# Kernel optimization log

Measured on AMD Instinct MI355X. Metric: run time of the kernel, lower is better.

The kernel has to match this reference:

```python
import jax, jax.numpy as jnp
import numpy as np

CS = 64          # chunk_size
CP = CS - 1      # causal_padding
H = 8            # heads
DH = 64          # dim_head
SCALE = DH ** -0.5


def rotate_half(x):
    x1, x2 = jnp.split(x, 2, axis=-1)
    return jnp.concatenate((-x2, x1), axis=-1)


def apply_rope(t, freqs):
    rd = freqs.shape[-1]
    t_rot, t_pass = t[..., :rd], t[..., rd:]
    t_rot = t_rot * jnp.cos(freqs) + rotate_half(t_rot) * jnp.sin(freqs)
    return jnp.concatenate((t_rot, t_pass), axis=-1)


def setup_inputs() -> dict:
    key = jax.random.key(0)
    ks = jax.random.split(key, 10)
    b, n, dim = 4, 4096, 1024
    k_chunks, r, rlen = 64, 2, 128
    inner = H * DH
    return {
        "x": jax.random.normal(ks[0], (b, n, dim), dtype=jnp.float32),
        "context": jax.random.normal(ks[1], (b, k_chunks, r, rlen, dim), dtype=jnp.float32),
        "q_pos_emb": jax.random.normal(ks[2], (1, 1, CS, DH), dtype=jnp.float32),
        "k_pos_emb": jax.random.normal(ks[3], (1, 1, rlen, DH), dtype=jnp.float32),
        "Wq": jax.random.normal(ks[4], (dim, inner), dtype=jnp.float32) * 0.02,
        "Wk": jax.random.normal(ks[5], (dim, inner), dtype=jnp.float32) * 0.02,
        "Wv": jax.random.normal(ks[6], (dim, inner), dtype=jnp.float32) * 0.02,
        "Wo": jax.random.normal(ks[7], (inner, dim), dtype=jnp.float32) * 0.02,
        "bo": jnp.zeros((dim,), dtype=jnp.float32),
        "null_k": jax.random.normal(ks[8], (inner,), dtype=jnp.float32),
        "null_v": jax.random.normal(ks[9], (inner,), dtype=jnp.float32),
    }


def reference(x, context, q_pos_emb, k_pos_emb, Wq, Wk, Wv, Wo, bo, null_k, null_v):
    b, n, dim = x.shape
    _, k_chunks, r, rlen, _ = context.shape
    # causal shift: drop first CP tokens, pad CP zeros at end (F.pad with -CP)
    xs = jnp.pad(x[:, CP:], ((0, 0), (0, CP), (0, 0)))
    seq_index = (n // CS) * CS
    rem = n - seq_index
    xs = xs[:, :seq_index]                                   # [b, k*CS, dim]
    # shift q rope the same way; pad region gets freqs=0 -> identity rotation
    qpe = jnp.pad(q_pos_emb[:, :, CP:], ((0, 0), (0, 0), (0, CP), (0, 0)))
    kpe = jnp.tile(k_pos_emb, (1, 1, r, 1))                  # [1,1,r*rlen,DH]
    bk = b * k_chunks
    xc = xs.reshape(bk, CS, dim)
    ctx = context.reshape(bk, r * rlen, dim)
    # projections -> [bk, h, seq, dh]
    q = (xc @ Wq).reshape(bk, CS, H, DH).transpose(0, 2, 1, 3) * SCALE
    k = (ctx @ Wk).reshape(bk, r * rlen, H, DH).transpose(0, 2, 1, 3)
    v = (ctx @ Wv).reshape(bk, r * rlen, H, DH).transpose(0, 2, 1, 3)
    q = apply_rope(q, qpe)
    k = apply_rope(k, kpe)
    # null kv prepend
    nk = jnp.broadcast_to(null_k.reshape(1, H, 1, DH), (bk, H, 1, DH))
    nv = jnp.broadcast_to(null_v.reshape(1, H, 1, DH), (bk, H, 1, DH))
    k = jnp.concatenate((nk, k), axis=2)
    v = jnp.concatenate((nv, v), axis=2)
    sim = jnp.einsum('bhid,bhjd->bhij', q, k)
    attn = jax.nn.softmax(sim, axis=-1)
    o = jnp.einsum('bhij,bhjd->bhid', attn, v)
    o = o.transpose(0, 2, 1, 3).reshape(bk, CS, H * DH)
    o = o @ Wo + bo                                          # [bk, CS, dim]
    o = o.reshape(b, k_chunks * CS, dim)
    # unshift: pad CP zeros at front, trim CP - rem from end
    o = jnp.concatenate(
        (jnp.zeros((b, CP, dim), o.dtype), o[:, :k_chunks * CS - CP + rem]), axis=1)
    return o
```

## Files before the change

### kernel.cpp

```cpp
#include <hip/hip_runtime.h>


#define DEV __device__ __forceinline__

typedef __bf16 bf16x8 __attribute__((ext_vector_type(8)));
typedef float f32x4 __attribute__((ext_vector_type(4)));

DEV unsigned short f2bf(float f) {
  union { float f; unsigned int u; } v; v.f = f;
  unsigned int u = v.u;
  unsigned int r = (u + 0x7FFFu + ((u >> 16) & 1u)) >> 16;
  return (unsigned short)r;
}
DEV float bf2f(unsigned short h) {
  union { unsigned int u; float f; } v; v.u = ((unsigned int)h) << 16;
  return v.f;
}
DEV unsigned int pkbf(unsigned int hi, unsigned int lo) {
  return __builtin_amdgcn_perm(hi, lo, 0x07060302u);
}

DEV void ldst16(const void* g, void* l) {
  __builtin_amdgcn_global_load_lds(
      (const __attribute__((address_space(1))) void*)g,
      (__attribute__((address_space(3))) void*)l, 16, 0, 0);
}

DEV void bar() { __builtin_amdgcn_s_barrier(); }
#define VMCNT4 asm volatile("s_waitcnt vmcnt(4)" ::: "memory")
#define VMCNT0 asm volatile("s_waitcnt vmcnt(0)" ::: "memory")

__global__ __launch_bounds__(256) void prep_k(const float* __restrict__ Wq,
                                              const float* __restrict__ Wk,
                                              const float* __restrict__ Wv,
                                              const float* __restrict__ Wo,
                                              const float* __restrict__ qpe,
                                              const float* __restrict__ kpe,
                                              unsigned short* __restrict__ Wqt,
                                              unsigned short* __restrict__ Wkt,
                                              unsigned short* __restrict__ Wvt,
                                              unsigned short* __restrict__ Wot,
                                              float* __restrict__ ck, float* __restrict__ sk,
                                              float* __restrict__ cq, float* __restrict__ sq,
                                              float* __restrict__ out) {
  __shared__ float tl[64][65];
  int blk = blockIdx.x;
  int tid = threadIdx.x;
  if (blk < 512) {
    int mat = blk >> 7, loc = blk & 127;
    const float* W;
    unsigned short* Wt;
    int R, C;
    float scale = 1.0f;
    if (mat == 0)      { W = Wq; Wt = Wqt; R = 1024; C = 512; scale = 0.125f; }
    else if (mat == 1) { W = Wk; Wt = Wkt; R = 1024; C = 512; }
    else if (mat == 2) { W = Wv; Wt = Wvt; R = 1024; C = 512; }
    else               { W = Wo; Wt = Wot; R = 512;  C = 1024; }
    int nct = C >> 6;
    int rt = loc / nct, ct = loc % nct;
    int r0 = rt << 6, c0 = ct << 6;
    #pragma unroll
    for (int i = 0; i < 16; ++i) {
      int flat = i * 256 + tid;
      int rr = flat >> 6, cc = flat & 63;
      tl[rr][cc] = W[(size_t)(r0 + rr) * C + c0 + cc] * scale;
    }
    __syncthreads();
    #pragma unroll
    for (int i = 0; i < 16; ++i) {
      int flat = i * 256 + tid;
      int cc = flat >> 6, rr = flat & 63;
      Wt[(size_t)(c0 + cc) * R + r0 + rr] = f2bf(tl[rr][cc]);
    }
  } else if (blk < 764) {
    int r = blk - 512;
    int b = r / 63, rr = r % 63;
    float4 z = {0.f, 0.f, 0.f, 0.f};
    *(float4*)(out + (((size_t)(b * 4096 + rr)) << 10) + tid * 4) = z;
  } else {
    int t = (blk - 764) * 256 + tid;
    float f = kpe[t];
    ck[t] = cosf(f);
    sk[t] = sinf(f);
    if (t < 64) {
      float g = qpe[63 * 64 + t];
      cq[t] = cosf(g);
      sq[t] = sinf(g);
    }
  }
}

__global__ __launch_bounds__(256) void cast_k(const float* __restrict__ src,
                                              unsigned short* __restrict__ dst) {
  size_t base = ((size_t)blockIdx.x * 256 + threadIdx.x) * 8;
  uint4 lo = *(const uint4*)(src + base);
  uint4 hi = *(const uint4*)(src + base + 4);
  uint4 pk;
  pk.x = pkbf(lo.y, lo.x);
  pk.y = pkbf(lo.w, lo.z);
  pk.z = pkbf(hi.y, hi.x);
  pk.w = pkbf(hi.w, hi.z);
  *(uint4*)(dst + base) = pk;
}

template <int MODE>
__global__ __launch_bounds__(256) void gemm_proj(const float* __restrict__ Af,
                                                 const unsigned short* __restrict__ B0,
                                                 const unsigned short* __restrict__ B1,
                                                 unsigned short* __restrict__ out0,
                                                 unsigned short* __restrict__ out1,
                                                 const float* __restrict__ ck,
                                                 const float* __restrict__ sk,
                                                 const float* __restrict__ cq,
                                                 const float* __restrict__ sq) {
  __shared__ unsigned short sh[16384];
  unsigned short* As = sh;
  unsigned short* Bs = sh + 8192;
  const int K = 1024;

  int id = blockIdx.x;
  int x, y, z;
  if (MODE == 0) { x = (id & 7) + 8 * (id >> 5); y = (id >> 3) & 3; z = 0; }
  else           { x = (id & 7) + 8 * (id >> 6); int j = (id >> 3) & 7; y = j & 3; z = j >> 2; }
  const unsigned short* B = z ? B1 : B0;
  int m0 = x * 128, n0 = y * 128;
  int tid = threadIdx.x, w = tid >> 6, lane = tid & 63;
  int wm = (w & 1) * 64, wn = (w >> 1) * 64;
  int Lrow = lane >> 3, Lc = lane & 7;
  int srcC = Lc ^ (Lrow & 7);

  const float* asrc[4];
  bool avalid[4];
  #pragma unroll
  for (int q = 0; q < 4; ++q) {
    int t = w * 4 + q;
    int gm = m0 + t * 8 + Lrow;
    if (MODE == 0) {
      int b = gm >> 12, p = gm & 4095;
      avalid[q] = (p <= 4032);
      asrc[q] = Af + (((size_t)(b << 12) + p + 63) << 10) + srcC * 8;
    } else {
      avalid[q] = true;
      asrc[q] = Af + (size_t)gm * 1024 + srcC * 8;
    }
  }

  f32x4 acc[4][4] = {};

  for (int k0 = 0; k0 < K; k0 += 64) {
    #pragma unroll
    for (int q = 0; q < 4; ++q) {
      int t = w * 4 + q;
      uint4 lo = {0, 0, 0, 0}, hi = {0, 0, 0, 0};
      if (avalid[q]) {
        lo = *(const uint4*)(asrc[q] + k0);
        hi = *(const uint4*)(asrc[q] + k0 + 4);
      }
      uint4 pk;
      pk.x = pkbf(lo.y, lo.x);
      pk.y = pkbf(lo.w, lo.z);
      pk.z = pkbf(hi.y, hi.x);
      pk.w = pkbf(hi.w, hi.z);
      *(uint4*)((char*)As + t * 1024 + lane * 16) = pk;
      ldst16(B + (size_t)(n0 + t * 8 + Lrow) * K + (k0 + srcC * 8), (char*)Bs + t * 1024);
    }
    __syncthreads();
    #pragma unroll
    for (int k32 = 0; k32 < 2; ++k32) {
      int c = k32 * 4 + (lane >> 4);
      bf16x8 af[4], bfr[4];
      #pragma unroll
      for (int mt = 0; mt < 4; ++mt) {
        int m = wm + mt * 16 + (lane & 15);
        af[mt] = *(const bf16x8*)((const char*)As + m * 128 + (c ^ (m & 7)) * 16);
      }
      #pragma unroll
      for (int nt = 0; nt < 4; ++nt) {
        int n = wn + nt * 16 + (lane & 15);
        bfr[nt] = *(const bf16x8*)((const char*)Bs + n * 128 + (c ^ (n & 7)) * 16);
      }
      #pragma unroll
      for (int mt = 0; mt < 4; ++mt)
        #pragma unroll
        for (int nt = 0; nt < 4; ++nt)
          acc[mt][nt] = __builtin_amdgcn_mfma_f32_16x16x32_bf16(af[mt], bfr[nt], acc[mt][nt], 0, 0, 0);
    }
    __syncthreads();
  }

  if (MODE == 0) {
    #pragma unroll
    for (int mt = 0; mt < 4; ++mt)
      #pragma unroll
      for (int nt = 0; nt < 4; ++nt)
        #pragma unroll
        for (int r = 0; r < 4; ++r) {
          int m = m0 + wm + mt * 16 + (lane >> 4) * 4 + r;
          int n = n0 + wn + nt * 16 + (lane & 15);
          float val = acc[mt][nt][r];
          if ((m & 63) == 0) {
            int d = nt * 16 + (lane & 15);
            float partner = acc[mt][nt ^ 2][r];
            val = val * cq[d] + (nt < 2 ? -partner : partner) * sq[d];
          }
          out0[(size_t)m * 512 + n] = f2bf(val);
        }
  } else if (z == 0) {
    #pragma unroll
    for (int mt = 0; mt < 4; ++mt)
      #pragma unroll
      for (int r = 0; r < 4; ++r) {
        int m = m0 + wm + mt * 16 + (lane >> 4) * 4 + r;
        int fib = (m & 127) * 64;
        #pragma unroll
        for (int nt = 0; nt < 4; ++nt) {
          int n = n0 + wn + nt * 16 + (lane & 15);
          int d = nt * 16 + (lane & 15);
          float partner = acc[mt][nt ^ 2][r];
          float val = acc[mt][nt][r] * ck[fib + d] + (nt < 2 ? -partner : partner) * sk[fib + d];
          out0[(size_t)m * 512 + n] = f2bf(val);
        }
      }
  } else {
    #pragma unroll
    for (int mt = 0; mt < 4; ++mt)
      #pragma unroll
      for (int nt = 0; nt < 4; ++nt)
        #pragma unroll
        for (int r = 0; r < 4; ++r) {
          int ml = wm + mt * 16 + (lane >> 4) * 4 + r;
          int nl = wn + nt * 16 + (lane & 15);
          int mc = ml >> 3, me = ml & 7;
          *(unsigned short*)((char*)sh + nl * 256 + ((mc ^ (nl & 15)) * 16) + me * 2) =
              f2bf(acc[mt][nt][r]);
        }
    __syncthreads();
    #pragma unroll
    for (int i = 0; i < 8; ++i) {
      int flat = i * 256 + tid;
      int nl = flat >> 4, mc = flat & 15;
      uint4 v = *(const uint4*)((const char*)sh + nl * 256 + ((mc ^ (nl & 15)) * 16));
      *(uint4*)(out1 + (size_t)(n0 + nl) * 65536 + m0 + mc * 8) = v;
    }
  }
}

DEV bf16x8 rdfrag(const unsigned short* b, int row, int c) {
  return *(const bf16x8*)((const char*)b + row * 128 + ((c ^ (row & 7)) << 4));
}

DEV void rdA(const unsigned short* bufA, int wm, int ln15, int l4, int mtb,
             bf16x8 (&af)[2][2]) {
  #pragma unroll
  for (int mq = 0; mq < 2; ++mq)
    #pragma unroll
    for (int kk = 0; kk < 2; ++kk)
      af[mq][kk] = rdfrag(bufA, wm + (mtb + mq) * 16 + ln15, kk * 4 + l4);
}

DEV void rdB(const unsigned short* bufB, int wn, int ln15, int l4, bf16x8 (&bf)[4][2]) {
  #pragma unroll
  for (int nt = 0; nt < 4; ++nt)
    #pragma unroll
    for (int kk = 0; kk < 2; ++kk)
      bf[nt][kk] = rdfrag(bufB, wn + nt * 16 + ln15, kk * 4 + l4);
}

template <int MTB>
DEV void mfma16(const bf16x8 (&af)[2][2], const bf16x8 (&bf)[4][2], f32x4 (&acc)[8][4]) {
  __builtin_amdgcn_s_setprio(1);
  #pragma unroll
  for (int mq = 0; mq < 2; ++mq)
    #pragma unroll
    for (int nt = 0; nt < 4; ++nt)
      #pragma unroll
      for (int kk = 0; kk < 2; ++kk)
        acc[MTB + mq][nt] = __builtin_amdgcn_mfma_f32_16x16x32_bf16(
            af[mq][kk], bf[nt][kk], acc[MTB + mq][nt], 0, 0, 0);
  __builtin_amdgcn_s_setprio(0);
}

DEV void stg(unsigned short* buf, const unsigned short* src, int r0, int w,
             int Lrow, int srcC, int k0, int h) {
  #pragma unroll
  for (int qq = 0; qq < 2; ++qq) {
    int q = 2 * h + qq;
    ldst16(src + (size_t)(r0 + q * 64 + w * 8 + Lrow) * 1024 + (k0 + srcC * 8),
           (char*)buf + ((q * 512 + w * 64) << 4));
  }
}

__global__ __launch_bounds__(512, 2) void gemm_kv(const unsigned short* __restrict__ Abf,
                                                  const unsigned short* __restrict__ Bk,
                                                  const unsigned short* __restrict__ Bv,
                                                  unsigned short* __restrict__ kb,
                                                  unsigned short* __restrict__ vtg,
                                                  const float* __restrict__ ck,
                                                  const float* __restrict__ sk,
                                                  int mbase) {
  __shared__ unsigned short sh[65536];
  unsigned short* A0b = sh;
  unsigned short* A1b = sh + 16384;
  unsigned short* B0b = sh + 32768;
  unsigned short* B1b = sh + 49152;

  int id = blockIdx.x;
  int x = (id & 7) + 8 * (id >> 5);
  int j = (id >> 3) & 3;
  int y = j & 1, z = j >> 1;
  const unsigned short* Bz = z ? Bv : Bk;
  int m0l = x << 8;
  int m0 = mbase + m0l;
  int n0 = y << 8;

  int tid = threadIdx.x, w = tid >> 6, lane = tid & 63;
  int wm = (w & 1) * 128, wn = (w >> 1) * 64;
  int ln15 = lane & 15, l4 = lane >> 4;
  int Lrow = lane >> 3;
  int srcC = (lane & 7) ^ (Lrow & 7);

  f32x4 acc[8][4] = {};

  stg(A0b, Abf, m0l, w, Lrow, srcC, 0, 0);
  stg(A0b, Abf, m0l, w, Lrow, srcC, 0, 1);
  stg(B0b, Bz, n0, w, Lrow, srcC, 0, 0);
  stg(B0b, Bz, n0, w, Lrow, srcC, 0, 1);
  stg(B1b, Bz, n0, w, Lrow, srcC, 64, 0);
  stg(B1b, Bz, n0, w, Lrow, srcC, 64, 1);
  VMCNT4;
  bar();

  for (int it = 0; it < 8; ++it) {
    const int k0 = it * 128;
    bf16x8 af[2][2], bf[4][2];

    rdB(B0b, wn, ln15, l4, bf);
    rdA(A0b, wm, ln15, l4, 0, af);
    stg(A1b, Abf, m0l, w, Lrow, srcC, k0 + 64, 0);
    bar(); mfma16<0>(af, bf, acc); bar();

    rdA(A0b, wm, ln15, l4, 2, af);
    stg(A1b, Abf, m0l, w, Lrow, srcC, k0 + 64, 1);
    bar(); mfma16<2>(af, bf, acc); bar();

    rdA(A0b, wm, ln15, l4, 4, af);
    stg(B0b, Bz, n0, w, Lrow, srcC, (k0 + 128) & 1023, 0);
    bar(); mfma16<4>(af, bf, acc); bar();

    rdA(A0b, wm, ln15, l4, 6, af);
    stg(B0b, Bz, n0, w, Lrow, srcC, (k0 + 128) & 1023, 1);
    VMCNT4;
    bar(); mfma16<6>(af, bf, acc); bar();

    rdB(B1b, wn, ln15, l4, bf);
    rdA(A1b, wm, ln15, l4, 0, af);
    stg(A0b, Abf, m0l, w, Lrow, srcC, (k0 + 128) & 1023, 0);
    bar(); mfma16<0>(af, bf, acc); bar();

    rdA(A1b, wm, ln15, l4, 2, af);
    stg(A0b, Abf, m0l, w, Lrow, srcC, (k0 + 128) & 1023, 1);
    bar(); mfma16<2>(af, bf, acc); bar();

    rdA(A1b, wm, ln15, l4, 4, af);
    stg(B1b, Bz, n0, w, Lrow, srcC, (k0 + 192) & 1023, 0);
    bar(); mfma16<4>(af, bf, acc); bar();

    rdA(A1b, wm, ln15, l4, 6, af);
    stg(B1b, Bz, n0, w, Lrow, srcC, (k0 + 192) & 1023, 1);
    VMCNT4;
    bar(); mfma16<6>(af, bf, acc); bar();
  }

  VMCNT0;
  bar();

  if (z == 0) {
    #pragma unroll
    for (int mt = 0; mt < 8; ++mt)
      #pragma unroll
      for (int r = 0; r < 4; ++r) {
        int m = m0 + wm + mt * 16 + l4 * 4 + r;
        int fib = (m & 127) << 6;
        #pragma unroll
        for (int nt = 0; nt < 4; ++nt) {
          int d = nt * 16 + ln15;
          float partner = acc[mt][nt ^ 2][r];
          float val = acc[mt][nt][r] * ck[fib + d] + (nt < 2 ? -partner : partner) * sk[fib + d];
          kb[(size_t)m * 512 + n0 + wn + d] = f2bf(val);
        }
      }
  } else {
    #pragma unroll
    for (int mt = 0; mt < 8; ++mt)
      #pragma unroll
      for (int nt = 0; nt < 4; ++nt)
        #pragma unroll
        for (int r = 0; r < 4; ++r) {
          int ml = wm + mt * 16 + l4 * 4 + r;
          int nl = wn + nt * 16 + ln15;
          int mc = ml >> 3, me = ml & 7;
          *(unsigned short*)((char*)sh + nl * 512 + ((mc ^ (nl & 31)) << 4) + me * 2) =
              f2bf(acc[mt][nt][r]);
        }
    __syncthreads();
    #pragma unroll
    for (int i = 0; i < 16; ++i) {
      int flat = i * 512 + tid;
      int nl = flat >> 5, mc = flat & 31;
      uint4 v = *(const uint4*)((const char*)sh + nl * 512 + ((mc ^ (nl & 31)) << 4));
      *(uint4*)(vtg + (size_t)(n0 + nl) * 65536 + m0 + mc * 8) = v;
    }
  }
}

__global__ __launch_bounds__(256) void gemm_out(const unsigned short* __restrict__ A,
                                                const unsigned short* __restrict__ B,
                                                const float* __restrict__ bias,
                                                float* __restrict__ out) {
  __shared__ unsigned short sh[16384];
  unsigned short* As = sh;
  unsigned short* Bs = sh + 8192;
  const int K = 512, N = 1024;
  int id = blockIdx.x;
  int x = (id & 7) + 8 * (id >> 6), y = (id >> 3) & 7;
  int m0 = x * 128, n0 = y * 128;
  int tid = threadIdx.x, w = tid >> 6, lane = tid & 63;
  int wm = (w & 1) * 64, wn = (w >> 1) * 64;
  int Lrow = lane >> 3, Lc = lane & 7;
  int srcC = Lc ^ (Lrow & 7);

  f32x4 acc[4][4] = {};

  for (int k0 = 0; k0 < K; k0 += 64) {
    #pragma unroll
    for (int q = 0; q < 4; ++q) {
      int t = w * 4 + q;
      ldst16(A + (size_t)(m0 + t * 8 + Lrow) * K + (k0 + srcC * 8), (char*)As + t * 1024);
      ldst16(B + (size_t)(n0 + t * 8 + Lrow) * K + (k0 + srcC * 8), (char*)Bs + t * 1024);
    }
    __syncthreads();
    #pragma unroll
    for (int k32 = 0; k32 < 2; ++k32) {
      int c = k32 * 4 + (lane >> 4);
      bf16x8 af[4], bfr[4];
      #pragma unroll
      for (int mt = 0; mt < 4; ++mt) {
        int m = wm + mt * 16 + (lane & 15);
        af[mt] = *(const bf16x8*)((const char*)As + m * 128 + (c ^ (m & 7)) * 16);
      }
      #pragma unroll
      for (int nt = 0; nt < 4; ++nt) {
        int n = wn + nt * 16 + (lane & 15);
        bfr[nt] = *(const bf16x8*)((const char*)Bs + n * 128 + (c ^ (n & 7)) * 16);
      }
      #pragma unroll
      for (int mt = 0; mt < 4; ++mt)
        #pragma unroll
        for (int nt = 0; nt < 4; ++nt)
          acc[mt][nt] = __builtin_amdgcn_mfma_f32_16x16x32_bf16(af[mt], bfr[nt], acc[mt][nt], 0, 0, 0);
    }
    __syncthreads();
  }
  #pragma unroll
  for (int mt = 0; mt < 4; ++mt)
    #pragma unroll
    for (int nt = 0; nt < 4; ++nt)
      #pragma unroll
      for (int r = 0; r < 4; ++r) {
        int m = m0 + wm + mt * 16 + (lane >> 4) * 4 + r;
        int n = n0 + wn + nt * 16 + (lane & 15);
        int b = m >> 12, t = m & 4095;
        if (t <= 4032)
          out[((size_t)((b << 12) + t + 63)) * N + n] = acc[mt][nt][r] + bias[n];
      }
}

__global__ __launch_bounds__(256) void attn_kernel(const unsigned short* __restrict__ qb,
                                                   const unsigned short* __restrict__ kb,
                                                   const unsigned short* __restrict__ vtg,
                                                   const float* __restrict__ nullk,
                                                   const float* __restrict__ nullv,
                                                   unsigned short* __restrict__ ob) {
  __shared__ unsigned short qs[64 * 64];
  __shared__ unsigned short ks[256 * 64];
  __shared__ unsigned short ps[64 * 256];
  __shared__ float rnull[64];
  __shared__ float rsum[64];
  int id = blockIdx.x;
  int bc = (id & 7) + 8 * (id >> 6);
  int h = (id >> 3) & 7;
  int tid = threadIdx.x, w = tid >> 6, lane = tid & 63;
  int Lrow = lane >> 3, Lc = lane & 7, srcC = Lc ^ (Lrow & 7);

  #pragma unroll
  for (int q8 = 0; q8 < 2; ++q8) {
    int t = w * 2 + q8;
    ldst16(qb + (size_t)(bc * 64 + t * 8 + Lrow) * 512 + h * 64 + srcC * 8, (char*)qs + t * 1024);
  }
  #pragma unroll
  for (int q8 = 0; q8 < 8; ++q8) {
    int t = w * 8 + q8;
    ldst16(kb + (size_t)(bc * 256 + t * 8 + Lrow) * 512 + h * 64 + srcC * 8, (char*)ks + t * 1024);
  }
  __syncthreads();

  {
    int rl = lane >> 2, part = lane & 3;
    int row = w * 16 + rl;
    float s = 0.f;
    #pragma unroll
    for (int e = 0; e < 16; ++e) {
      int d = part * 16 + e;
      unsigned short qv = *(const unsigned short*)((const char*)qs + row * 128 +
                                                   (((d >> 3) ^ (row & 7)) * 16) + (d & 7) * 2);
      s += bf2f(qv) * nullk[h * 64 + d];
    }
    s += __shfl_xor(s, 1);
    s += __shfl_xor(s, 2);
    if (part == 0) rnull[row] = __expf(s);
  }

  f32x4 acc[16] = {};
  #pragma unroll
  for (int k32 = 0; k32 < 2; ++k32) {
    int c = k32 * 4 + (lane >> 4);
    int m = w * 16 + (lane & 15);
    bf16x8 a = *(const bf16x8*)((const char*)qs + m * 128 + (c ^ (m & 7)) * 16);
    #pragma unroll
    for (int nt = 0; nt < 16; ++nt) {
      int n = nt * 16 + (lane & 15);
      bf16x8 b = *(const bf16x8*)((const char*)ks + n * 128 + (c ^ (n & 7)) * 16);
      acc[nt] = __builtin_amdgcn_mfma_f32_16x16x32_bf16(a, b, acc[nt], 0, 0, 0);
    }
  }

  int g = lane >> 4;
  #pragma unroll
  for (int r = 0; r < 4; ++r) {
    int row = w * 16 + g * 4 + r;
    float s = 0.f;
    #pragma unroll
    for (int nt = 0; nt < 16; ++nt) {
      float p = __expf(acc[nt][r]);
      acc[nt][r] = p;
      s += p;
    }
    s += __shfl_xor(s, 1);
    s += __shfl_xor(s, 2);
    s += __shfl_xor(s, 4);
    s += __shfl_xor(s, 8);
    if ((lane & 15) == 0) rsum[row] = s + rnull[row];
  }

  #pragma unroll
  for (int nt = 0; nt < 16; ++nt)
    #pragma unroll
    for (int r = 0; r < 4; ++r) {
      int row = w * 16 + g * 4 + r;
      int col = nt * 16 + (lane & 15);
      *(unsigned short*)((char*)ps + row * 512 + (((col >> 3) ^ (row & 7)) * 16) + (col & 7) * 2) =
          f2bf(acc[nt][r]);
    }
  __syncthreads();

  #pragma unroll
  for (int q8 = 0; q8 < 8; ++q8) {
    int t = w * 8 + q8;
    int dd = t * 2 + (lane >> 5);
    int cl = (lane & 31) ^ (dd & 7);
    ldst16(vtg + (size_t)(h * 64 + dd) * 65536 + bc * 256 + cl * 8, (char*)ks + t * 1024);
  }
  __syncthreads();

  f32x4 oacc[4] = {};
  #pragma unroll
  for (int k32 = 0; k32 < 8; ++k32) {
    int c = k32 * 4 + (lane >> 4);
    int m = w * 16 + (lane & 15);
    bf16x8 a = *(const bf16x8*)((const char*)ps + m * 512 + (c ^ (m & 7)) * 16);
    #pragma unroll
    for (int nt = 0; nt < 4; ++nt) {
      int n = nt * 16 + (lane & 15);
      bf16x8 b = *(const bf16x8*)((const char*)ks + n * 512 + (c ^ (n & 7)) * 16);
      oacc[nt] = __builtin_amdgcn_mfma_f32_16x16x32_bf16(a, b, oacc[nt], 0, 0, 0);
    }
  }
  #pragma unroll
  for (int nt = 0; nt < 4; ++nt)
    #pragma unroll
    for (int r = 0; r < 4; ++r) {
      int row = w * 16 + g * 4 + r;
      int d = nt * 16 + (lane & 15);
      float o = oacc[nt][r] + rnull[row] * nullv[h * 64 + d];
      o /= rsum[row];
      ob[((size_t)(bc * 64 + row) * 8 + h) * 64 + d] = f2bf(o);
    }
}

extern "C" void kernel_launch(void* const* d_in, const int* in_sizes, int n_in,
                              void* d_out, int out_size, void* d_ws, size_t ws_size,
                              hipStream_t stream) {
  const float* x = (const float*)d_in[0];
  const float* ctx = (const float*)d_in[1];
  const float* qpe = (const float*)d_in[2];
  const float* kpe = (const float*)d_in[3];
  const float* Wq = (const float*)d_in[4];
  const float* Wk = (const float*)d_in[5];
  const float* Wv = (const float*)d_in[6];
  const float* Wo = (const float*)d_in[7];
  const float* bo = (const float*)d_in[8];
  const float* nk = (const float*)d_in[9];
  const float* nv = (const float*)d_in[10];
  float* out = (float*)d_out;
  char* ws = (char*)d_ws;

  unsigned short* Wqt  = (unsigned short*)(ws + 0);
  unsigned short* Wkt  = (unsigned short*)(ws + 1048576);
  unsigned short* Wvt  = (unsigned short*)(ws + 2097152);
  unsigned short* Wot  = (unsigned short*)(ws + 3145728);
  float* cosk = (float*)(ws + 4194304);
  float* sink = (float*)(ws + 4227072);
  float* cosq = (float*)(ws + 4259840);
  float* sinq = (float*)(ws + 4260096);
  unsigned short* qb   = (unsigned short*)(ws + 4260352);
  unsigned short* kb   = (unsigned short*)(ws + 21037568);
  unsigned short* vtg  = (unsigned short*)(ws + 88146432);
  unsigned short* obuf = (unsigned short*)(ws + 155255296);
  unsigned short* ctxb = (unsigned short*)(ws + 155255296);

  prep_k<<<796, 256, 0, stream>>>(Wq, Wk, Wv, Wo, qpe, kpe, Wqt, Wkt, Wvt, Wot,
                                  cosk, sink, cosq, sinq, out);

  gemm_proj<0><<<512, 256, 0, stream>>>(x, Wqt, Wqt, qb, nullptr,
                                        cosk, sink, cosq, sinq);

  cast_k<<<16384, 256, 0, stream>>>(ctx, ctxb);
  gemm_kv<<<512, 512, 0, stream>>>(ctxb, Wkt, Wvt, kb, vtg, cosk, sink, 0);
  cast_k<<<16384, 256, 0, stream>>>(ctx + 33554432, ctxb);
  gemm_kv<<<512, 512, 0, stream>>>(ctxb, Wkt, Wvt, kb, vtg, cosk, sink, 32768);

  attn_kernel<<<2048, 256, 0, stream>>>(qb, kb, vtg, nk, nv, obuf);

  gemm_out<<<1024, 256, 0, stream>>>(obuf, Wot, bo, out);
}
```

Baseline: 708.5 us.

## Merge Q/K/V projections into one pipelined GEMM and restructure attention

Casts all of context and shifted x to bf16 in one kernel. Q, K and V projections then run in a single launch that uses the double-buffered 256x256 tile loop from the old K/V GEMM, and the output projection moves to that same loop, replacing the smaller 128x128 single-buffer GEMMs. The attention kernel is reorganised so each lane owns one query row: it computes K·Q transposed, keeps the row sum and null-key terms in registers instead of shared memory, stages V in its own buffer, and writes packed outputs. This trades the extra bf16 staging traffic for x and all of context at once, plus a larger workspace, for fewer launches and better MFMA pipelining.

```diff
diff --git a/kernel.cpp b/kernel.cpp
--- a/kernel.cpp
+++ b/kernel.cpp
@@ -16,8 +16,15 @@
   union { unsigned int u; float f; } v; v.u = ((unsigned int)h) << 16;
   return v.f;
 }
+DEV float bfelem(bf16x8 v, int i) {
+  union { bf16x8 v; unsigned short u[8]; } t; t.v = v;
+  return bf2f(t.u[i]);
+}
 DEV unsigned int pkbf(unsigned int hi, unsigned int lo) {
   return __builtin_amdgcn_perm(hi, lo, 0x07060302u);
+}
+DEV unsigned int pk2(float lo, float hi) {
+  return ((unsigned int)f2bf(hi) << 16) | f2bf(lo);
 }
 
 DEV void ldst16(const void* g, void* l) {
@@ -90,163 +97,44 @@
   }
 }
 
-__global__ __launch_bounds__(256) void cast_k(const float* __restrict__ src,
-                                              unsigned short* __restrict__ dst) {
-  size_t base = ((size_t)blockIdx.x * 256 + threadIdx.x) * 8;
-  uint4 lo = *(const uint4*)(src + base);
-  uint4 hi = *(const uint4*)(src + base + 4);
-  uint4 pk;
-  pk.x = pkbf(lo.y, lo.x);
-  pk.y = pkbf(lo.w, lo.z);
-  pk.z = pkbf(hi.y, hi.x);
-  pk.w = pkbf(hi.w, hi.z);
-  *(uint4*)(dst + base) = pk;
-}
-
-template <int MODE>
-__global__ __launch_bounds__(256) void gemm_proj(const float* __restrict__ Af,
-                                                 const unsigned short* __restrict__ B0,
-                                                 const unsigned short* __restrict__ B1,
-                                                 unsigned short* __restrict__ out0,
-                                                 unsigned short* __restrict__ out1,
-                                                 const float* __restrict__ ck,
-                                                 const float* __restrict__ sk,
-                                                 const float* __restrict__ cq,
-                                                 const float* __restrict__ sq) {
-  __shared__ unsigned short sh[16384];
-  unsigned short* As = sh;
-  unsigned short* Bs = sh + 8192;
-  const int K = 1024;
-
+__global__ __launch_bounds__(256) void cast_all(const float* __restrict__ ctx,
+                                                const float* __restrict__ x,
+                                                unsigned short* __restrict__ ctxb,
+                                                unsigned short* __restrict__ xb) {
   int id = blockIdx.x;
-  int x, y, z;
-  if (MODE == 0) { x = (id & 7) + 8 * (id >> 5); y = (id >> 3) & 3; z = 0; }
-  else           { x = (id & 7) + 8 * (id >> 6); int j = (id >> 3) & 7; y = j & 3; z = j >> 2; }
-  const unsigned short* B = z ? B1 : B0;
-  int m0 = x * 128, n0 = y * 128;
-  int tid = threadIdx.x, w = tid >> 6, lane = tid & 63;
-  int wm = (w & 1) * 64, wn = (w >> 1) * 64;
-  int Lrow = lane >> 3, Lc = lane & 7;
-  int srcC = Lc ^ (Lrow & 7);
-
-  const float* asrc[4];
-  bool avalid[4];
-  #pragma unroll
-  for (int q = 0; q < 4; ++q) {
-    int t = w * 4 + q;
-    int gm = m0 + t * 8 + Lrow;
-    if (MODE == 0) {
-      int b = gm >> 12, p = gm & 4095;
-      avalid[q] = (p <= 4032);
-      asrc[q] = Af + (((size_t)(b << 12) + p + 63) << 10) + srcC * 8;
-    } else {
-      avalid[q] = true;
-      asrc[q] = Af + (size_t)gm * 1024 + srcC * 8;
-    }
-  }
-
-  f32x4 acc[4][4] = {};
-
-  for (int k0 = 0; k0 < K; k0 += 64) {
-    #pragma unroll
-    for (int q = 0; q < 4; ++q) {
-      int t = w * 4 + q;
-      uint4 lo = {0, 0, 0, 0}, hi = {0, 0, 0, 0};
-      if (avalid[q]) {
-        lo = *(const uint4*)(asrc[q] + k0);
-        hi = *(const uint4*)(asrc[q] + k0 + 4);
-      }
-      uint4 pk;
+  if (id < 32768) {
+    size_t base = ((size_t)id * 256 + threadIdx.x) * 8;
+    uint4 lo = *(const uint4*)(ctx + base);
+    uint4 hi = *(const uint4*)(ctx + base + 4);
+    uint4 pk;
+    pk.x = pkbf(lo.y, lo.x);
+    pk.y = pkbf(lo.w, lo.z);
+    pk.z = pkbf(hi.y, hi.x);
+    pk.w = pkbf(hi.w, hi.z);
+    *(uint4*)(ctxb + base) = pk;
+  } else {
+    size_t e = ((size_t)(id - 32768) * 256 + threadIdx.x) * 8;
+    int m = (int)(e >> 10), c = (int)(e & 1023);
+    int b = m >> 12, t = m & 4095;
+    uint4 pk = {0, 0, 0, 0};
+    if (t <= 4032) {
+      const float* s = x + (((size_t)(b << 12) + t + 63) << 10) + c;
+      uint4 lo = *(const uint4*)s;
+      uint4 hi = *(const uint4*)(s + 4);
       pk.x = pkbf(lo.y, lo.x);
       pk.y = pkbf(lo.w, lo.z);
       pk.z = pkbf(hi.y, hi.x);
       pk.w = pkbf(hi.w, hi.z);
-      *(uint4*)((char*)As + t * 1024 + lane * 16) = pk;
-      ldst16(B + (size_t)(n0 + t * 8 + Lrow) * K + (k0 + srcC * 8), (char*)Bs + t * 1024);
-    }
-    __syncthreads();
-    #pragma unroll
-    for (int k32 = 0; k32 < 2; ++k32) {
-      int c = k32 * 4 + (lane >> 4);
-      bf16x8 af[4], bfr[4];
-      #pragma unroll
-      for (int mt = 0; mt < 4; ++mt) {
-        int m = wm + mt * 16 + (lane & 15);
-        af[mt] = *(const bf16x8*)((const char*)As + m * 128 + (c ^ (m & 7)) * 16);
-      }
-      #pragma unroll
-      for (int nt = 0; nt < 4; ++nt) {
-        int n = wn + nt * 16 + (lane & 15);
-        bfr[nt] = *(const bf16x8*)((const char*)Bs + n * 128 + (c ^ (n & 7)) * 16);
-      }
-      #pragma unroll
-      for (int mt = 0; mt < 4; ++mt)
-        #pragma unroll
-        for (int nt = 0; nt < 4; ++nt)
-          acc[mt][nt] = __builtin_amdgcn_mfma_f32_16x16x32_bf16(af[mt], bfr[nt], acc[mt][nt], 0, 0, 0);
-    }
-    __syncthreads();
-  }
-
-  if (MODE == 0) {
-    #pragma unroll
-    for (int mt = 0; mt < 4; ++mt)
-      #pragma unroll
-      for (int nt = 0; nt < 4; ++nt)
-        #pragma unroll
-        for (int r = 0; r < 4; ++r) {
-          int m = m0 + wm + mt * 16 + (lane >> 4) * 4 + r;
-          int n = n0 + wn + nt * 16 + (lane & 15);
-          float val = acc[mt][nt][r];
-          if ((m & 63) == 0) {
-            int d = nt * 16 + (lane & 15);
-            float partner = acc[mt][nt ^ 2][r];
-            val = val * cq[d] + (nt < 2 ? -partner : partner) * sq[d];
-          }
-          out0[(size_t)m * 512 + n] = f2bf(val);
-        }
-  } else if (z == 0) {
-    #pragma unroll
-    for (int mt = 0; mt < 4; ++mt)
-      #pragma unroll
-      for (int r = 0; r < 4; ++r) {
-        int m = m0 + wm + mt * 16 + (lane >> 4) * 4 + r;
-        int fib = (m & 127) * 64;
-        #pragma unroll
-        for (int nt = 0; nt < 4; ++nt) {
-          int n = n0 + wn + nt * 16 + (lane & 15);
-          int d = nt * 16 + (lane & 15);
-          float partner = acc[mt][nt ^ 2][r];
-          float val = acc[mt][nt][r] * ck[fib + d] + (nt < 2 ? -partner : partner) * sk[fib + d];
-          out0[(size_t)m * 512 + n] = f2bf(val);
-        }
-      }
-  } else {
-    #pragma unroll
-    for (int mt = 0; mt < 4; ++mt)
-      #pragma unroll
-      for (int nt = 0; nt < 4; ++nt)
-        #pragma unroll
-        for (int r = 0; r < 4; ++r) {
-          int ml = wm + mt * 16 + (lane >> 4) * 4 + r;
-          int nl = wn + nt * 16 + (lane & 15);
-          int mc = ml >> 3, me = ml & 7;
-          *(unsigned short*)((char*)sh + nl * 256 + ((mc ^ (nl & 15)) * 16) + me * 2) =
-              f2bf(acc[mt][nt][r]);
-        }
-    __syncthreads();
-    #pragma unroll
-    for (int i = 0; i < 8; ++i) {
-      int flat = i * 256 + tid;
-      int nl = flat >> 4, mc = flat & 15;
-      uint4 v = *(const uint4*)((const char*)sh + nl * 256 + ((mc ^ (nl & 15)) * 16));
-      *(uint4*)(out1 + (size_t)(n0 + nl) * 65536 + m0 + mc * 8) = v;
-    }
+    }
+    *(uint4*)(xb + e) = pk;
   }
 }
 
 DEV bf16x8 rdfrag(const unsigned short* b, int row, int c) {
   return *(const bf16x8*)((const char*)b + row * 128 + ((c ^ (row & 7)) << 4));
+}
+DEV bf16x8 rdfrag512(const unsigned short* b, int row, int c) {
+  return *(const bf16x8*)((const char*)b + row * 512 + ((c ^ (row & 7)) << 4));
 }
 
 DEV void rdA(const unsigned short* bufA, int wm, int ln15, int l4, int mtb,
@@ -281,100 +169,122 @@
 }
 
 DEV void stg(unsigned short* buf, const unsigned short* src, int r0, int w,
-             int Lrow, int srcC, int k0, int h) {
+             int Lrow, int srcC, int k0, int h, int ldK) {
   #pragma unroll
   for (int qq = 0; qq < 2; ++qq) {
     int q = 2 * h + qq;
-    ldst16(src + (size_t)(r0 + q * 64 + w * 8 + Lrow) * 1024 + (k0 + srcC * 8),
+    ldst16(src + (size_t)(r0 + q * 64 + w * 8 + Lrow) * ldK + (k0 + srcC * 8),
            (char*)buf + ((q * 512 + w * 64) << 4));
   }
 }
 
-__global__ __launch_bounds__(512, 2) void gemm_kv(const unsigned short* __restrict__ Abf,
-                                                  const unsigned short* __restrict__ Bk,
-                                                  const unsigned short* __restrict__ Bv,
-                                                  unsigned short* __restrict__ kb,
-                                                  unsigned short* __restrict__ vtg,
-                                                  const float* __restrict__ ck,
-                                                  const float* __restrict__ sk,
-                                                  int mbase) {
-  __shared__ unsigned short sh[65536];
+template <int KD>
+DEV void kloop8(const unsigned short* __restrict__ A, const unsigned short* __restrict__ B,
+                unsigned short* sh, f32x4 (&acc)[8][4], int m0, int n0, int tid) {
   unsigned short* A0b = sh;
   unsigned short* A1b = sh + 16384;
   unsigned short* B0b = sh + 32768;
   unsigned short* B1b = sh + 49152;
-
-  int id = blockIdx.x;
-  int x = (id & 7) + 8 * (id >> 5);
-  int j = (id >> 3) & 3;
-  int y = j & 1, z = j >> 1;
-  const unsigned short* Bz = z ? Bv : Bk;
-  int m0l = x << 8;
-  int m0 = mbase + m0l;
-  int n0 = y << 8;
-
-  int tid = threadIdx.x, w = tid >> 6, lane = tid & 63;
+  int w = tid >> 6, lane = tid & 63;
   int wm = (w & 1) * 128, wn = (w >> 1) * 64;
   int ln15 = lane & 15, l4 = lane >> 4;
   int Lrow = lane >> 3;
   int srcC = (lane & 7) ^ (Lrow & 7);
-
-  f32x4 acc[8][4] = {};
-
-  stg(A0b, Abf, m0l, w, Lrow, srcC, 0, 0);
-  stg(A0b, Abf, m0l, w, Lrow, srcC, 0, 1);
-  stg(B0b, Bz, n0, w, Lrow, srcC, 0, 0);
-  stg(B0b, Bz, n0, w, Lrow, srcC, 0, 1);
-  stg(B1b, Bz, n0, w, Lrow, srcC, 64, 0);
-  stg(B1b, Bz, n0, w, Lrow, srcC, 64, 1);
+  const int MSK = KD - 1;
+
+  stg(A0b, A, m0, w, Lrow, srcC, 0, 0, KD);
+  stg(A0b, A, m0, w, Lrow, srcC, 0, 1, KD);
+  stg(B0b, B, n0, w, Lrow, srcC, 0, 0, KD);
+  stg(B0b, B, n0, w, Lrow, srcC, 0, 1, KD);
+  stg(B1b, B, n0, w, Lrow, srcC, 64, 0, KD);
+  stg(B1b, B, n0, w, Lrow, srcC, 64, 1, KD);
   VMCNT4;
   bar();
 
-  for (int it = 0; it < 8; ++it) {
+  for (int it = 0; it < KD / 128; ++it) {
     const int k0 = it * 128;
     bf16x8 af[2][2], bf[4][2];
 
     rdB(B0b, wn, ln15, l4, bf);
     rdA(A0b, wm, ln15, l4, 0, af);
-    stg(A1b, Abf, m0l, w, Lrow, srcC, k0 + 64, 0);
+    stg(A1b, A, m0, w, Lrow, srcC, k0 + 64, 0, KD);
     bar(); mfma16<0>(af, bf, acc); bar();
 
     rdA(A0b, wm, ln15, l4, 2, af);
-    stg(A1b, Abf, m0l, w, Lrow, srcC, k0 + 64, 1);
+    stg(A1b, A, m0, w, Lrow, srcC, k0 + 64, 1, KD);
     bar(); mfma16<2>(af, bf, acc); bar();
 
     rdA(A0b, wm, ln15, l4, 4, af);
-    stg(B0b, Bz, n0, w, Lrow, srcC, (k0 + 128) & 1023, 0);
+    stg(B0b, B, n0, w, Lrow, srcC, (k0 + 128) & MSK, 0, KD);
     bar(); mfma16<4>(af, bf, acc); bar();
 
     rdA(A0b, wm, ln15, l4, 6, af);
-    stg(B0b, Bz, n0, w, Lrow, srcC, (k0 + 128) & 1023, 1);
+    stg(B0b, B, n0, w, Lrow, srcC, (k0 + 128) & MSK, 1, KD);
     VMCNT4;
     bar(); mfma16<6>(af, bf, acc); bar();
 
     rdB(B1b, wn, ln15, l4, bf);
     rdA(A1b, wm, ln15, l4, 0, af);
-    stg(A0b, Abf, m0l, w, Lrow, srcC, (k0 + 128) & 1023, 0);
+    stg(A0b, A, m0, w, Lrow, srcC, (k0 + 128) & MSK, 0, KD);
     bar(); mfma16<0>(af, bf, acc); bar();
 
     rdA(A1b, wm, ln15, l4, 2, af);
-    stg(A0b, Abf, m0l, w, Lrow, srcC, (k0 + 128) & 1023, 1);
+    stg(A0b, A, m0, w, Lrow, srcC, (k0 + 128) & MSK, 1, KD);
     bar(); mfma16<2>(af, bf, acc); bar();
 
     rdA(A1b, wm, ln15, l4, 4, af);
-    stg(B1b, Bz, n0, w, Lrow, srcC, (k0 + 192) & 1023, 0);
+    stg(B1b, B, n0, w, Lrow, srcC, (k0 + 192) & MSK, 0, KD);
     bar(); mfma16<4>(af, bf, acc); bar();
 
     rdA(A1b, wm, ln15, l4, 6, af);
-    stg(B1b, Bz, n0, w, Lrow, srcC, (k0 + 192) & 1023, 1);
+    stg(B1b, B, n0, w, Lrow, srcC, (k0 + 192) & MSK, 1, KD);
     VMCNT4;
     bar(); mfma16<6>(af, bf, acc); bar();
   }
 
   VMCNT0;
   bar();
-
-  if (z == 0) {
+}
+
+__global__ __launch_bounds__(512, 2) void proj8(const unsigned short* __restrict__ ctxb,
+                                                const unsigned short* __restrict__ xb,
+                                                const unsigned short* __restrict__ Wkt,
+                                                const unsigned short* __restrict__ Wvt,
+                                                const unsigned short* __restrict__ Wqt,
+                                                unsigned short* __restrict__ kb,
+                                                unsigned short* __restrict__ vtg,
+                                                unsigned short* __restrict__ qbuf,
+                                                const float* __restrict__ ck,
+                                                const float* __restrict__ sk,
+                                                const float* __restrict__ cq,
+                                                const float* __restrict__ sq) {
+  __shared__ unsigned short sh[65536];
+  int id = blockIdx.x;
+  int mode, m0, n0;
+  const unsigned short *A, *B;
+  if (id < 1024) {
+    int x = (id & 7) + 8 * (id >> 5);
+    int j = (id >> 3) & 3;
+    int y = j & 1, z = j >> 1;
+    mode = z;
+    A = ctxb; B = z ? Wvt : Wkt;
+    m0 = x << 8; n0 = y << 8;
+  } else {
+    int t = id - 1024;
+    int x = (t & 7) + 8 * (t >> 4);
+    int y = (t >> 3) & 1;
+    mode = 2;
+    A = xb; B = Wqt;
+    m0 = x << 8; n0 = y << 8;
+  }
+  int tid = threadIdx.x, w = tid >> 6, lane = tid & 63;
+  int wm = (w & 1) * 128, wn = (w >> 1) * 64;
+  int ln15 = lane & 15, l4 = lane >> 4;
+
+  f32x4 acc[8][4] = {};
+  kloop8<1024>(A, B, sh, acc, m0, n0, tid);
+
+  if (mode == 0) {
     #pragma unroll
     for (int mt = 0; mt < 8; ++mt)
       #pragma unroll
@@ -389,7 +299,7 @@
           kb[(size_t)m * 512 + n0 + wn + d] = f2bf(val);
         }
       }
-  } else {
+  } else if (mode == 1) {
     #pragma unroll
     for (int mt = 0; mt < 8; ++mt)
       #pragma unroll
@@ -410,68 +320,53 @@
       uint4 v = *(const uint4*)((const char*)sh + nl * 512 + ((mc ^ (nl & 31)) << 4));
       *(uint4*)(vtg + (size_t)(n0 + nl) * 65536 + m0 + mc * 8) = v;
     }
-  }
-}
-
-__global__ __launch_bounds__(256) void gemm_out(const unsigned short* __restrict__ A,
-                                                const unsigned short* __restrict__ B,
-                                                const float* __restrict__ bias,
-                                                float* __restrict__ out) {
-  __shared__ unsigned short sh[16384];
-  unsigned short* As = sh;
-  unsigned short* Bs = sh + 8192;
-  const int K = 512, N = 1024;
+  } else {
+    #pragma unroll
+    for (int mt = 0; mt < 8; ++mt)
+      #pragma unroll
+      for (int nt = 0; nt < 4; ++nt)
+        #pragma unroll
+        for (int r = 0; r < 4; ++r) {
+          int m = m0 + wm + mt * 16 + l4 * 4 + r;
+          int n = n0 + wn + nt * 16 + ln15;
+          float val = acc[mt][nt][r];
+          if ((m & 63) == 0) {
+            int d = nt * 16 + ln15;
+            float partner = acc[mt][nt ^ 2][r];
+            val = val * cq[d] + (nt < 2 ? -partner : partner) * sq[d];
+          }
+          qbuf[(size_t)m * 512 + n] = f2bf(val);
+        }
+  }
+}
+
+__global__ __launch_bounds__(512, 2) void out8(const unsigned short* __restrict__ A,
+                                               const unsigned short* __restrict__ B,
+                                               const float* __restrict__ bias,
+                                               float* __restrict__ out) {
+  __shared__ unsigned short sh[65536];
   int id = blockIdx.x;
-  int x = (id & 7) + 8 * (id >> 6), y = (id >> 3) & 7;
-  int m0 = x * 128, n0 = y * 128;
+  int x = (id & 7) + 8 * (id >> 5);
+  int y = (id >> 3) & 3;
+  int m0 = x << 8, n0 = y << 8;
   int tid = threadIdx.x, w = tid >> 6, lane = tid & 63;
-  int wm = (w & 1) * 64, wn = (w >> 1) * 64;
-  int Lrow = lane >> 3, Lc = lane & 7;
-  int srcC = Lc ^ (Lrow & 7);
-
-  f32x4 acc[4][4] = {};
-
-  for (int k0 = 0; k0 < K; k0 += 64) {
-    #pragma unroll
-    for (int q = 0; q < 4; ++q) {
-      int t = w * 4 + q;
-      ldst16(A + (size_t)(m0 + t * 8 + Lrow) * K + (k0 + srcC * 8), (char*)As + t * 1024);
-      ldst16(B + (size_t)(n0 + t * 8 + Lrow) * K + (k0 + srcC * 8), (char*)Bs + t * 1024);
-    }
-    __syncthreads();
-    #pragma unroll
-    for (int k32 = 0; k32 < 2; ++k32) {
-      int c = k32 * 4 + (lane >> 4);
-      bf16x8 af[4], bfr[4];
-      #pragma unroll
-      for (int mt = 0; mt < 4; ++mt) {
-        int m = wm + mt * 16 + (lane & 15);
-        af[mt] = *(const bf16x8*)((const char*)As + m * 128 + (c ^ (m & 7)) * 16);
-      }
-      #pragma unroll
-      for (int nt = 0; nt < 4; ++nt) {
-        int n = wn + nt * 16 + (lane & 15);
-        bfr[nt] = *(const bf16x8*)((const char*)Bs + n * 128 + (c ^ (n & 7)) * 16);
-      }
-      #pragma unroll
-      for (int mt = 0; mt < 4; ++mt)
-        #pragma unroll
-        for (int nt = 0; nt < 4; ++nt)
-          acc[mt][nt] = __builtin_amdgcn_mfma_f32_16x16x32_bf16(af[mt], bfr[nt], acc[mt][nt], 0, 0, 0);
-    }
-    __syncthreads();
-  }
-  #pragma unroll
-  for (int mt = 0; mt < 4; ++mt)
+  int wm = (w & 1) * 128, wn = (w >> 1) * 64;
+  int ln15 = lane & 15, l4 = lane >> 4;
+
+  f32x4 acc[8][4] = {};
+  kloop8<512>(A, B, sh, acc, m0, n0, tid);
+
+  #pragma unroll
+  for (int mt = 0; mt < 8; ++mt)
     #pragma unroll
     for (int nt = 0; nt < 4; ++nt)
       #pragma unroll
       for (int r = 0; r < 4; ++r) {
-        int m = m0 + wm + mt * 16 + (lane >> 4) * 4 + r;
-        int n = n0 + wn + nt * 16 + (lane & 15);
+        int m = m0 + wm + mt * 16 + l4 * 4 + r;
+        int n = n0 + wn + nt * 16 + ln15;
         int b = m >> 12, t = m & 4095;
         if (t <= 4032)
-          out[((size_t)((b << 12) + t + 63)) * N + n] = acc[mt][nt][r] + bias[n];
+          out[((size_t)((b << 12) + t + 63)) * 1024 + n] = acc[mt][nt][r] + bias[n];
       }
 }
 
@@ -483,14 +378,13 @@
                                                    unsigned short* __restrict__ ob) {
   __shared__ unsigned short qs[64 * 64];
   __shared__ unsigned short ks[256 * 64];
-  __shared__ unsigned short ps[64 * 256];
-  __shared__ float rnull[64];
-  __shared__ float rsum[64];
+  __shared__ unsigned short vs[64 * 256];
   int id = blockIdx.x;
   int bc = (id & 7) + 8 * (id >> 6);
   int h = (id >> 3) & 7;
   int tid = threadIdx.x, w = tid >> 6, lane = tid & 63;
-  int Lrow = lane >> 3, Lc = lane & 7, srcC = Lc ^ (Lrow & 7);
+  int ln15 = lane & 15, l4 = lane >> 4;
+  int Lrow = lane >> 3, srcC = (lane & 7) ^ (Lrow & 7);
 
   #pragma unroll
   for (int q8 = 0; q8 < 2; ++q8) {
@@ -502,99 +396,92 @@
     int t = w * 8 + q8;
     ldst16(kb + (size_t)(bc * 256 + t * 8 + Lrow) * 512 + h * 64 + srcC * 8, (char*)ks + t * 1024);
   }
-  __syncthreads();
-
-  {
-    int rl = lane >> 2, part = lane & 3;
-    int row = w * 16 + rl;
-    float s = 0.f;
-    #pragma unroll
-    for (int e = 0; e < 16; ++e) {
-      int d = part * 16 + e;
-      unsigned short qv = *(const unsigned short*)((const char*)qs + row * 128 +
-                                                   (((d >> 3) ^ (row & 7)) * 16) + (d & 7) * 2);
-      s += bf2f(qv) * nullk[h * 64 + d];
-    }
-    s += __shfl_xor(s, 1);
-    s += __shfl_xor(s, 2);
-    if (part == 0) rnull[row] = __expf(s);
-  }
-
-  f32x4 acc[16] = {};
-  #pragma unroll
-  for (int k32 = 0; k32 < 2; ++k32) {
-    int c = k32 * 4 + (lane >> 4);
-    int m = w * 16 + (lane & 15);
-    bf16x8 a = *(const bf16x8*)((const char*)qs + m * 128 + (c ^ (m & 7)) * 16);
-    #pragma unroll
-    for (int nt = 0; nt < 16; ++nt) {
-      int n = nt * 16 + (lane & 15);
-      bf16x8 b = *(const bf16x8*)((const char*)ks + n * 128 + (c ^ (n & 7)) * 16);
-      acc[nt] = __builtin_amdgcn_mfma_f32_16x16x32_bf16(a, b, acc[nt], 0, 0, 0);
-    }
-  }
-
-  int g = lane >> 4;
-  #pragma unroll
-  for (int r = 0; r < 4; ++r) {
-    int row = w * 16 + g * 4 + r;
-    float s = 0.f;
-    #pragma unroll
-    for (int nt = 0; nt < 16; ++nt) {
-      float p = __expf(acc[nt][r]);
-      acc[nt][r] = p;
-      s += p;
-    }
-    s += __shfl_xor(s, 1);
-    s += __shfl_xor(s, 2);
-    s += __shfl_xor(s, 4);
-    s += __shfl_xor(s, 8);
-    if ((lane & 15) == 0) rsum[row] = s + rnull[row];
-  }
-
-  #pragma unroll
-  for (int nt = 0; nt < 16; ++nt)
-    #pragma unroll
-    for (int r = 0; r < 4; ++r) {
-      int row = w * 16 + g * 4 + r;
-      int col = nt * 16 + (lane & 15);
-      *(unsigned short*)((char*)ps + row * 512 + (((col >> 3) ^ (row & 7)) * 16) + (col & 7) * 2) =
-          f2bf(acc[nt][r]);
-    }
-  __syncthreads();
-
   #pragma unroll
   for (int q8 = 0; q8 < 8; ++q8) {
     int t = w * 8 + q8;
     int dd = t * 2 + (lane >> 5);
     int cl = (lane & 31) ^ (dd & 7);
-    ldst16(vtg + (size_t)(h * 64 + dd) * 65536 + bc * 256 + cl * 8, (char*)ks + t * 1024);
+    ldst16(vtg + (size_t)(h * 64 + dd) * 65536 + bc * 256 + cl * 8, (char*)vs + t * 1024);
   }
   __syncthreads();
 
+  int q = w * 16 + ln15;
+
+  float ns = 0.f;
+  {
+    bf16x8 q0 = rdfrag(qs, q, l4 * 2);
+    bf16x8 q1 = rdfrag(qs, q, l4 * 2 + 1);
+    const float* nkp = nullk + h * 64 + l4 * 16;
+    #pragma unroll
+    for (int i = 0; i < 8; ++i) ns += bfelem(q0, i) * nkp[i];
+    #pragma unroll
+    for (int i = 0; i < 8; ++i) ns += bfelem(q1, i) * nkp[8 + i];
+    ns += __shfl_xor(ns, 16);
+    ns += __shfl_xor(ns, 32);
+  }
+  float rnull = __expf(ns);
+
+  f32x4 acc[16] = {};
+  #pragma unroll
+  for (int k32 = 0; k32 < 2; ++k32) {
+    int c = k32 * 4 + l4;
+    bf16x8 bq = rdfrag(qs, q, c);
+    #pragma unroll
+    for (int nt = 0; nt < 16; ++nt) {
+      bf16x8 ak = rdfrag(ks, nt * 16 + ln15, c);
+      acc[nt] = __builtin_amdgcn_mfma_f32_16x16x32_bf16(ak, bq, acc[nt], 0, 0, 0);
+    }
+  }
+
+  float s = 0.f;
+  #pragma unroll
+  for (int nt = 0; nt < 16; ++nt)
+    #pragma unroll
+    for (int r = 0; r < 4; ++r) {
+      float p = __expf(acc[nt][r]);
+      acc[nt][r] = p;
+      s += p;
+    }
+  s += __shfl_xor(s, 16);
+  s += __shfl_xor(s, 32);
+  float rsum = s + rnull;
+
+  __syncthreads();
+
+  #pragma unroll
+  for (int nt = 0; nt < 16; ++nt) {
+    unsigned int w0 = pk2(acc[nt][0], acc[nt][1]);
+    unsigned int w1 = pk2(acc[nt][2], acc[nt][3]);
+    int j = nt * 16 + l4 * 4;
+    int cj = j >> 3;
+    int off = (j & 7) * 2;
+    uint2 v = {w0, w1};
+    *(uint2*)((char*)ks + q * 512 + ((cj ^ (q & 7)) << 4) + off) = v;
+  }
   f32x4 oacc[4] = {};
   #pragma unroll
-  for (int k32 = 0; k32 < 8; ++k32) {
-    int c = k32 * 4 + (lane >> 4);
-    int m = w * 16 + (lane & 15);
-    bf16x8 a = *(const bf16x8*)((const char*)ps + m * 512 + (c ^ (m & 7)) * 16);
+  for (int kk = 0; kk < 8; ++kk) {
+    int c = kk * 4 + l4;
+    bf16x8 bp = rdfrag512(ks, q, c);
     #pragma unroll
     for (int nt = 0; nt < 4; ++nt) {
-      int n = nt * 16 + (lane & 15);
-      bf16x8 b = *(const bf16x8*)((const char*)ks + n * 512 + (c ^ (n & 7)) * 16);
-      oacc[nt] = __builtin_amdgcn_mfma_f32_16x16x32_bf16(a, b, oacc[nt], 0, 0, 0);
-    }
-  }
-  #pragma unroll
-  for (int nt = 0; nt < 4; ++nt)
-    #pragma unroll
-    for (int r = 0; r < 4; ++r) {
-      int row = w * 16 + g * 4 + r;
-      int d = nt * 16 + (lane & 15);
-      float o = oacc[nt][r] + rnull[row] * nullv[h * 64 + d];
-      o /= rsum[row];
-      ob[((size_t)(bc * 64 + row) * 8 + h) * 64 + d] = f2bf(o);
-    }
+      bf16x8 av = rdfrag512(vs, nt * 16 + ln15, c);
+      oacc[nt] = __builtin_amdgcn_mfma_f32_16x16x32_bf16(av, bp, oacc[nt], 0, 0, 0);
+    }
+  }
+
+  float inv = 1.0f / rsum;
+  #pragma unroll
+  for (int nt = 0; nt < 4; ++nt) {
+    const float* nvp = nullv + h * 64 + nt * 16 + l4 * 4;
+    float4 nv4 = *(const float4*)nvp;
+    float o0 = (oacc[nt][0] + rnull * nv4.x) * inv;
+    float o1 = (oacc[nt][1] + rnull * nv4.y) * inv;
+    float o2 = (oacc[nt][2] + rnull * nv4.z) * inv;
+    float o3 = (oacc[nt][3] + rnull * nv4.w) * inv;
+    uint2 v = {pk2(o0, o1), pk2(o2, o3)};
+    *(uint2*)(ob + ((size_t)(bc * 64 + q) * 8 + h) * 64 + nt * 16 + l4 * 4) = v;
+  }
 }
 
 extern "C" void kernel_launch(void* const* d_in, const int* in_sizes, int n_in,
@@ -622,24 +509,22 @@
   float* sink = (float*)(ws + 4227072);
   float* cosq = (float*)(ws + 4259840);
   float* sinq = (float*)(ws + 4260096);
-  unsigned short* qb   = (unsigned short*)(ws + 4260352);
-  unsigned short* kb   = (unsigned short*)(ws + 21037568);
-  unsigned short* vtg  = (unsigned short*)(ws + 88146432);
-  unsigned short* obuf = (unsigned short*)(ws + 155255296);
-  unsigned short* ctxb = (unsigned short*)(ws + 155255296);
+  unsigned short* qb   = (unsigned short*)(ws + 8388608);
+  unsigned short* kb   = (unsigned short*)(ws + 25165824);
+  unsigned short* vtg  = (unsigned short*)(ws + 92274688);
+  unsigned short* obuf = (unsigned short*)(ws + 159383552);
+  unsigned short* xb   = (unsigned short*)(ws + 176160768);
+  unsigned short* ctxb = (unsigned short*)(ws + 209715200);
 
   prep_k<<<796, 256, 0, stream>>>(Wq, Wk, Wv, Wo, qpe, kpe, Wqt, Wkt, Wvt, Wot,
                                   cosk, sink, cosq, sinq, out);
 
-  gemm_proj<0><<<512, 256, 0, stream>>>(x, Wqt, Wqt, qb, nullptr,
-                                        cosk, sink, cosq, sinq);
-
-  cast_k<<<16384, 256, 0, stream>>>(ctx, ctxb);
-  gemm_kv<<<512, 512, 0, stream>>>(ctxb, Wkt, Wvt, kb, vtg, cosk, sink, 0);
-  cast_k<<<16384, 256, 0, stream>>>(ctx + 33554432, ctxb);
-  gemm_kv<<<512, 512, 0, stream>>>(ctxb, Wkt, Wvt, kb, vtg, cosk, sink, 32768);
+  cast_all<<<40960, 256, 0, stream>>>(ctx, x, ctxb, xb);
+
+  proj8<<<1152, 512, 0, stream>>>(ctxb, xb, Wkt, Wvt, Wqt, kb, vtg, qb,
+                                  cosk, sink, cosq, sinq);
 
   attn_kernel<<<2048, 256, 0, stream>>>(qb, kb, vtg, nk, nv, obuf);
 
-  gemm_out<<<1024, 256, 0, stream>>>(obuf, Wot, bo, out);
-}
+  out8<<<256, 512, 0, stream>>>(obuf, Wot, bo, out);
+}
```

Result: faster. 673.8 us (-4.9%).
